# Kernel optimization log

Hardware: AMD Instinct MI355X
Metric: run time of the kernel (lower is better)

Reference implementation:

```python
import jax, jax.numpy as jnp
import numpy as np

VX, VY = 0.2, 0.2
X_OFF = VX / 2 + 0.0      # pc_range x_min = 0
Y_OFF = VY / 2 + (-40.0)  # pc_range y_min = -40
BN_EPS = 1e-3


def setup_inputs() -> dict:
    key = jax.random.key(0)
    k1, k2, k3, k4, k5, k6 = jax.random.split(key, 6)
    K, P, C_IN, C_AUG, C_OUT = 20000, 100, 4, 9, 64
    features = jax.random.normal(k1, (K, P, C_IN), dtype=jnp.float32)
    # at least 1 point per pillar (avoids div-by-zero, as in real voxelization)
    num_voxels = jax.random.randint(k2, (K,), 1, P + 1, dtype=jnp.int64)
    coors = jax.random.randint(k3, (K, 4), 0, 352, dtype=jnp.int64)
    W = jax.random.normal(k4, (C_AUG, C_OUT), dtype=jnp.float32) * (1.0 / np.sqrt(C_AUG))
    gamma = jnp.ones((C_OUT,), dtype=jnp.float32) + 0.1 * jax.random.normal(k5, (C_OUT,), dtype=jnp.float32)
    beta = 0.1 * jax.random.normal(k6, (C_OUT,), dtype=jnp.float32)
    return {"features": features, "num_voxels": num_voxels, "coors": coors,
            "W": W, "gamma": gamma, "beta": beta}


def reference(features, num_voxels, coors, W, gamma, beta):
    K, P, _ = features.shape
    dt = features.dtype
    pn = num_voxels.astype(dt)[:, None, None]                      # [K,1,1]
    cx = coors[:, 3].astype(dt)[:, None] * VX + X_OFF              # [K,1]
    cy = coors[:, 2].astype(dt)[:, None] * VY + Y_OFF              # [K,1]
    mask = (jnp.arange(P)[None, :] < num_voxels[:, None]).astype(dt)[..., None]  # [K,P,1]
    # cluster offset: point xyz minus per-pillar mean
    points_mean = features[..., :3].sum(axis=-2, keepdims=True) / pn
    f_cluster = features[..., :3] - points_mean                    # [K,P,3]
    # center offset: point xy minus pillar center
    f_center = jnp.stack([features[..., 0] - cx, features[..., 1] - cy], axis=-1)  # [K,P,2]
    feats = jnp.concatenate([features, f_cluster, f_center], axis=-1) * mask       # [K,P,9]
    # PFNLayer: Linear(no bias) -> BatchNorm1d (training-mode batch stats) -> ReLU -> max over points
    x = jnp.einsum('kpc,cu->kpu', feats, W)                        # [K,P,64]
    mu = x.mean(axis=(0, 1))
    var = ((x - mu) ** 2).mean(axis=(0, 1))
    x = (x - mu) * jax.lax.rsqrt(var + BN_EPS) * gamma + beta
    x = jax.nn.relu(x)
    return x.max(axis=1)                                           # [K,64] (squeezed)
```

## Files before the change

kernel.cpp:

```cpp
#include <hip/hip_runtime.h>


#define NBA 1252
#define NBB 64

__device__ __forceinline__ float wred63(float v) {
  int t;
  t = __builtin_amdgcn_update_dpp(0, __float_as_int(v), 0xB1, 0xf, 0xf, true);
  v += __int_as_float(t);
  t = __builtin_amdgcn_update_dpp(0, __float_as_int(v), 0x4E, 0xf, 0xf, true);
  v += __int_as_float(t);
  t = __builtin_amdgcn_update_dpp(0, __float_as_int(v), 0x141, 0xf, 0xf, true);
  v += __int_as_float(t);
  t = __builtin_amdgcn_update_dpp(0, __float_as_int(v), 0x140, 0xf, 0xf, true);
  v += __int_as_float(t);
  t = __builtin_amdgcn_update_dpp(0, __float_as_int(v), 0x142, 0xa, 0xf, true);
  v += __int_as_float(t);
  t = __builtin_amdgcn_update_dpp(0, __float_as_int(v), 0x143, 0xc, 0xf, true);
  v += __int_as_float(t);
  return v;
}

__device__ __forceinline__ float wred_add(float v) {
  int t;
  t = __builtin_amdgcn_update_dpp(0, __float_as_int(v), 0xB1, 0xf, 0xf, true);
  v += __int_as_float(t);
  t = __builtin_amdgcn_update_dpp(0, __float_as_int(v), 0x4E, 0xf, 0xf, true);
  v += __int_as_float(t);
  t = __builtin_amdgcn_update_dpp(0, __float_as_int(v), 0x141, 0xf, 0xf, true);
  v += __int_as_float(t);
  t = __builtin_amdgcn_update_dpp(0, __float_as_int(v), 0x140, 0xf, 0xf, true);
  v += __int_as_float(t);
  v += __shfl_xor(v, 16, 64);
  v += __shfl_xor(v, 32, 64);
  return v;
}

__global__ void __launch_bounds__(512) pfn_main(
    const float4* __restrict__ feat, const int* __restrict__ nvox, int K,
    int P, int cnt, const float* __restrict__ W,
    const float* __restrict__ gamma, float* __restrict__ pA,
    float4* __restrict__ ext, float4* __restrict__ rec) {
  __shared__ float4 pts[8][108];
  __shared__ float red[8][10];
  const int lane = threadIdx.x & 63;
  const int wid = threadIdx.x >> 6;
  const int q = lane & 15;
  const int g = lane >> 4;

  const float4* Wq = (const float4*)W;
  const float4 g4 = ((const float4*)gamma)[q];
  float4 sg;
  sg.x = (g4.x >= 0.f) ? 1.f : -1.f;
  sg.y = (g4.y >= 0.f) ? 1.f : -1.f;
  sg.z = (g4.z >= 0.f) ? 1.f : -1.f;
  sg.w = (g4.w >= 0.f) ? 1.f : -1.f;
  const float4 a0 = Wq[0 * 16 + q], a1 = Wq[1 * 16 + q], a2 = Wq[2 * 16 + q];
  const float4 a3 = Wq[3 * 16 + q], a4 = Wq[4 * 16 + q], a5 = Wq[5 * 16 + q];
  const float4 a6 = Wq[6 * 16 + q], a7 = Wq[7 * 16 + q], a8 = Wq[8 * 16 + q];
  float4 wx, wy, wz, w3;
  wx.x = (a0.x + a4.x + a7.x) * sg.x; wx.y = (a0.y + a4.y + a7.y) * sg.y;
  wx.z = (a0.z + a4.z + a7.z) * sg.z; wx.w = (a0.w + a4.w + a7.w) * sg.w;
  wy.x = (a1.x + a5.x + a8.x) * sg.x; wy.y = (a1.y + a5.y + a8.y) * sg.y;
  wy.z = (a1.z + a5.z + a8.z) * sg.z; wy.w = (a1.w + a5.w + a8.w) * sg.w;
  wz.x = (a2.x + a6.x) * sg.x; wz.y = (a2.y + a6.y) * sg.y;
  wz.z = (a2.z + a6.z) * sg.z; wz.w = (a2.w + a6.w) * sg.w;
  w3.x = a3.x * sg.x; w3.y = a3.y * sg.y;
  w3.z = a3.z * sg.z; w3.w = a3.w * sg.w;

  float q2[10] = {0, 0, 0, 0, 0, 0, 0, 0, 0, 0};

  const int gw = blockIdx.x * 8 + wid;
  const int k0 = gw * cnt;
  const int kend = (k0 + cnt < K) ? k0 + cnt : K;
  const bool hih = lane < (P - 64);

  for (int k = k0; k < kend; ++k) {
    const size_t base = (size_t)k * P;
    const float4 f0 = feat[base + lane];
    float4 f1;
    if (hih) f1 = feat[base + 64 + lane];
    const int nv = nvox[k];

    pts[wid][lane] = f0;
    if (hih) pts[wid][64 + lane] = f1;

    float sax = f0.x, say = f0.y, saz = f0.z;
    float svx = 0, svy = 0, svz = 0, svw = 0;
    if (lane < nv) {
      svx = f0.x; svy = f0.y; svz = f0.z; svw = f0.w;
      q2[0] = fmaf(f0.x, f0.x, q2[0]); q2[1] = fmaf(f0.x, f0.y, q2[1]);
      q2[2] = fmaf(f0.x, f0.z, q2[2]); q2[3] = fmaf(f0.x, f0.w, q2[3]);
      q2[4] = fmaf(f0.y, f0.y, q2[4]); q2[5] = fmaf(f0.y, f0.z, q2[5]);
      q2[6] = fmaf(f0.y, f0.w, q2[6]); q2[7] = fmaf(f0.z, f0.z, q2[7]);
      q2[8] = fmaf(f0.z, f0.w, q2[8]); q2[9] = fmaf(f0.w, f0.w, q2[9]);
    }
    if (hih) {
      sax += f1.x; say += f1.y; saz += f1.z;
      if (64 + lane < nv) {
        svx += f1.x; svy += f1.y; svz += f1.z; svw += f1.w;
        q2[0] = fmaf(f1.x, f1.x, q2[0]); q2[1] = fmaf(f1.x, f1.y, q2[1]);
        q2[2] = fmaf(f1.x, f1.z, q2[2]); q2[3] = fmaf(f1.x, f1.w, q2[3]);
        q2[4] = fmaf(f1.y, f1.y, q2[4]); q2[5] = fmaf(f1.y, f1.z, q2[5]);
        q2[6] = fmaf(f1.y, f1.w, q2[6]); q2[7] = fmaf(f1.z, f1.z, q2[7]);
        q2[8] = fmaf(f1.z, f1.w, q2[8]); q2[9] = fmaf(f1.w, f1.w, q2[9]);
      }
    }

    const float rx = wred63(sax), ry = wred63(say), rz = wred63(saz);
    const float vx = wred63(svx), vy = wred63(svy);
    const float vz = wred63(svz), vw = wred63(svw);

    float4 m4 = {-3e38f, -3e38f, -3e38f, -3e38f};
    int p = 0;
    for (; p + 8 <= nv; p += 8) {
      const float4 fa = pts[wid][p + g];
      const float4 fb = pts[wid][p + 4 + g];
      m4.x = fmaxf(m4.x, fmaf(fa.x, wx.x, fmaf(fa.y, wy.x, fmaf(fa.z, wz.x, fa.w * w3.x))));
      m4.y = fmaxf(m4.y, fmaf(fa.x, wx.y, fmaf(fa.y, wy.y, fmaf(fa.z, wz.y, fa.w * w3.y))));
      m4.z = fmaxf(m4.z, fmaf(fa.x, wx.z, fmaf(fa.y, wy.z, fmaf(fa.z, wz.z, fa.w * w3.z))));
      m4.w = fmaxf(m4.w, fmaf(fa.x, wx.w, fmaf(fa.y, wy.w, fmaf(fa.z, wz.w, fa.w * w3.w))));
      m4.x = fmaxf(m4.x, fmaf(fb.x, wx.x, fmaf(fb.y, wy.x, fmaf(fb.z, wz.x, fb.w * w3.x))));
      m4.y = fmaxf(m4.y, fmaf(fb.x, wx.y, fmaf(fb.y, wy.y, fmaf(fb.z, wz.y, fb.w * w3.y))));
      m4.z = fmaxf(m4.z, fmaf(fb.x, wx.z, fmaf(fb.y, wy.z, fmaf(fb.z, wz.z, fb.w * w3.z))));
      m4.w = fmaxf(m4.w, fmaf(fb.x, wx.w, fmaf(fb.y, wy.w, fmaf(fb.z, wz.w, fb.w * w3.w))));
    }
    if (p < nv) {
      const int i0 = p + g, i1 = p + 4 + g;
      const float4 fa = pts[wid][i0];
      const float4 fb = pts[wid][i1];
      if (i0 < nv) {
        m4.x = fmaxf(m4.x, fmaf(fa.x, wx.x, fmaf(fa.y, wy.x, fmaf(fa.z, wz.x, fa.w * w3.x))));
        m4.y = fmaxf(m4.y, fmaf(fa.x, wx.y, fmaf(fa.y, wy.y, fmaf(fa.z, wz.y, fa.w * w3.y))));
        m4.z = fmaxf(m4.z, fmaf(fa.x, wx.z, fmaf(fa.y, wy.z, fmaf(fa.z, wz.z, fa.w * w3.z))));
        m4.w = fmaxf(m4.w, fmaf(fa.x, wx.w, fmaf(fa.y, wy.w, fmaf(fa.z, wz.w, fa.w * w3.w))));
      }
      if (i1 < nv) {
        m4.x = fmaxf(m4.x, fmaf(fb.x, wx.x, fmaf(fb.y, wy.x, fmaf(fb.z, wz.x, fb.w * w3.x))));
        m4.y = fmaxf(m4.y, fmaf(fb.x, wx.y, fmaf(fb.y, wy.y, fmaf(fb.z, wz.y, fb.w * w3.y))));
        m4.z = fmaxf(m4.z, fmaf(fb.x, wx.z, fmaf(fb.y, wy.z, fmaf(fb.z, wz.z, fb.w * w3.z))));
        m4.w = fmaxf(m4.w, fmaf(fb.x, wx.w, fmaf(fb.y, wy.w, fmaf(fb.z, wz.w, fb.w * w3.w))));
      }
    }
    m4.x = fmaxf(m4.x, __shfl_xor(m4.x, 16, 64));
    m4.y = fmaxf(m4.y, __shfl_xor(m4.y, 16, 64));
    m4.z = fmaxf(m4.z, __shfl_xor(m4.z, 16, 64));
    m4.w = fmaxf(m4.w, __shfl_xor(m4.w, 16, 64));
    m4.x = fmaxf(m4.x, __shfl_xor(m4.x, 32, 64));
    m4.y = fmaxf(m4.y, __shfl_xor(m4.y, 32, 64));
    m4.z = fmaxf(m4.z, __shfl_xor(m4.z, 32, 64));
    m4.w = fmaxf(m4.w, __shfl_xor(m4.w, 32, 64));

    if (lane < 16) ext[(size_t)k * 16 + q] = m4;
    if (lane == 63) {
      float4 r0; r0.x = vx; r0.y = vy; r0.z = vz; r0.w = vw;
      float4 r1; r1.x = rx; r1.y = ry; r1.z = rz; r1.w = (float)nv;
      rec[2 * (size_t)k] = r0;
      rec[2 * (size_t)k + 1] = r1;
    }
  }

#pragma unroll
  for (int i = 0; i < 10; ++i) q2[i] = wred63(q2[i]);
  if (lane == 63) {
#pragma unroll
    for (int i = 0; i < 10; ++i) red[wid][i] = q2[i];
  }
  __syncthreads();
  const int t = threadIdx.x;
  if (t < 10) {
    float s = 0.f;
#pragma unroll
    for (int w = 0; w < 8; ++w) s += red[w][t];
    pA[t * NBA + blockIdx.x] = s;
  }
}

__global__ void __launch_bounds__(256) pfn_cross(
    const float4* __restrict__ rec, const int* __restrict__ coors, int K,
    float* __restrict__ pB) {
  __shared__ float red[4][44];
  const int lane = threadIdx.x & 63;
  const int wid = threadIdx.x >> 6;
  float q1[4] = {0, 0, 0, 0};
  float S[20];
  float u1[5] = {0, 0, 0, 0, 0};
  float u2[15];
#pragma unroll
  for (int i = 0; i < 20; ++i) S[i] = 0.f;
#pragma unroll
  for (int i = 0; i < 15; ++i) u2[i] = 0.f;

  for (int k = blockIdx.x * 256 + threadIdx.x; k < K; k += NBB * 256) {
    const float4 sv = rec[2 * (size_t)k];
    const float4 rb = rec[2 * (size_t)k + 1];
    const float nvf = rb.w, inv = 1.f / nvf;
    const float cx = (float)coors[k * 4 + 3] * 0.2f + 0.1f;
    const float cy = (float)coors[k * 4 + 2] * 0.2f - 39.9f;
    const float o[5] = {-rb.x * inv, -rb.y * inv, -rb.z * inv, -cx, -cy};
    const float s4[4] = {sv.x, sv.y, sv.z, sv.w};
#pragma unroll
    for (int a = 0; a < 4; ++a) q1[a] += s4[a];
#pragma unroll
    for (int a = 0; a < 4; ++a)
#pragma unroll
      for (int b = 0; b < 5; ++b)
        S[a * 5 + b] = fmaf(s4[a], o[b], S[a * 5 + b]);
    float no[5];
#pragma unroll
    for (int b = 0; b < 5; ++b) { no[b] = nvf * o[b]; u1[b] += no[b]; }
    int ui = 0;
#pragma unroll
    for (int b = 0; b < 5; ++b)
#pragma unroll
      for (int b2 = b; b2 < 5; ++b2) {
        u2[ui] = fmaf(no[b], o[b2], u2[ui]);
        ++ui;
      }
  }

  float a44[44];
#pragma unroll
  for (int i = 0; i < 4; ++i) a44[i] = q1[i];
#pragma unroll
  for (int i = 0; i < 20; ++i) a44[4 + i] = S[i];
#pragma unroll
  for (int i = 0; i < 5; ++i) a44[24 + i] = u1[i];
#pragma unroll
  for (int i = 0; i < 15; ++i) a44[29 + i] = u2[i];
#pragma unroll
  for (int i = 0; i < 44; ++i) a44[i] = wred_add(a44[i]);
  if (lane == 0) {
#pragma unroll
    for (int i = 0; i < 44; ++i) red[wid][i] = a44[i];
  }
  __syncthreads();
  const int t = threadIdx.x;
  if (t < 44)
    pB[t * NBB + blockIdx.x] =
        red[0][t] + red[1][t] + red[2][t] + red[3][t];
}

__global__ void __launch_bounds__(256) pfn_finalize(
    const float* __restrict__ pA, const float* __restrict__ pB,
    const float* __restrict__ W, const float* __restrict__ gamma,
    const float* __restrict__ beta, float invN, float* __restrict__ ss) {
  __shared__ float msum[54];
  __shared__ float m54[54];
  const int t = threadIdx.x;
  const int r = t >> 2, j = t & 3;
  if (r < 54) {
    const float* row;
    int nb;
    if (r >= 4 && r < 14) { row = pA + (size_t)(r - 4) * NBA; nb = NBA; }
    else {
      const int br = (r < 4) ? r : (r - 10);
      row = pB + (size_t)br * NBB;
      nb = NBB;
    }
    const int chunk = nb >> 2;
    row += j * chunk;
    float a0 = 0, a1 = 0, a2 = 0, a3 = 0, a4 = 0, a5 = 0, a6 = 0, a7 = 0;
    int b = 0;
    for (; b + 8 <= chunk; b += 8) {
      a0 += row[b];     a1 += row[b + 1]; a2 += row[b + 2]; a3 += row[b + 3];
      a4 += row[b + 4]; a5 += row[b + 5]; a6 += row[b + 6]; a7 += row[b + 7];
    }
    for (; b < chunk; ++b) a0 += row[b];
    float s = ((a0 + a1) + (a2 + a3)) + ((a4 + a5) + (a6 + a7));
    s += __shfl_xor(s, 1, 64);
    s += __shfl_xor(s, 2, 64);
    if (j == 0) msum[r] = s;
  }
  __syncthreads();
  if (t < 54) {
    float v;
    if (t < 9) {
      const int g = (t < 4) ? t : (t < 7 ? t - 4 : t - 7);
      v = msum[g];
      if (t >= 4) v += msum[34 + (t - 4)];
    } else {
      int r2 = t - 9, c = 0;
      while (r2 >= 9 - c) { r2 -= 9 - c; ++c; }
      const int c2 = c + r2;
      const int a = (c < 4) ? c : (c < 7 ? c - 4 : c - 7);
      const int b2 = (c2 < 4) ? c2 : (c2 < 7 ? c2 - 4 : c2 - 7);
      const int lo = a < b2 ? a : b2, hi = a < b2 ? b2 : a;
      v = msum[4 + lo * (9 - lo) / 2 + (hi - lo)];
      if (c2 >= 4) v += msum[14 + a * 5 + (c2 - 4)];
      if (c >= 4) v += msum[14 + b2 * 5 + (c - 4)];
      if (c >= 4 && c2 >= 4) {
        const int ua = c - 4, ub = c2 - 4;
        v += msum[39 + ua * 5 - ua * (ua - 1) / 2 + (ub - ua)];
      }
    }
    m54[t] = v;
  }
  __syncthreads();
  if (t < 64) {
    float wc[9];
#pragma unroll
    for (int c = 0; c < 9; ++c) wc[c] = W[c * 64 + t];
    float mu = 0.f;
#pragma unroll
    for (int c = 0; c < 9; ++c) mu += m54[c] * invN * wc[c];
    float ex2 = 0.f;
    int idx = 9;
#pragma unroll
    for (int c = 0; c < 9; ++c)
#pragma unroll
      for (int c2 = c; c2 < 9; ++c2) {
        float v = m54[idx] * invN * wc[c] * wc[c2];
        ex2 += (c == c2) ? v : 2.f * v;
        ++idx;
      }
    const float var = ex2 - mu * mu;
    const float scale = gamma[t] * rsqrtf(var + 1e-3f);
    ss[t] = scale;
    ss[64 + t] = beta[t] - mu * scale;
  }
}

__global__ void __launch_bounds__(256) pfn_apply(
    const float4* __restrict__ ext, const float4* __restrict__ rec,
    const int* __restrict__ coors, const float* __restrict__ W,
    const float* __restrict__ ss, int K, int P, float4* __restrict__ out) {
  const int t = blockIdx.x * 256 + threadIdx.x;
  if (t >= K * 16) return;
  const int k = t >> 4, j = t & 15;

  const float4* Wq = (const float4*)W;
  const float4 v4 = Wq[4 * 16 + j], v5 = Wq[5 * 16 + j];
  const float4 v6 = Wq[6 * 16 + j], v7 = Wq[7 * 16 + j];
  const float4 v8 = Wq[8 * 16 + j];

  const float4 e = ext[t];
  const float4 rb = rec[2 * (size_t)k + 1];
  const float nvf = rb.w, inv = 1.f / nvf;
  const float cx = (float)coors[k * 4 + 3] * 0.2f + 0.1f;
  const float cy = (float)coors[k * 4 + 2] * 0.2f - 39.9f;
  const float o0 = -rb.x * inv, o1 = -rb.y * inv, o2 = -rb.z * inv;
  float4 bias;
  bias.x = v4.x * o0 + v5.x * o1 + v6.x * o2 - v7.x * cx - v8.x * cy;
  bias.y = v4.y * o0 + v5.y * o1 + v6.y * o2 - v7.y * cx - v8.y * cy;
  bias.z = v4.z * o0 + v5.z * o1 + v6.z * o2 - v7.z * cx - v8.z * cy;
  bias.w = v4.w * o0 + v5.w * o1 + v6.w * o2 - v7.w * cx - v8.w * cy;

  const float4 sc = ((const float4*)ss)[j];
  const float4 sh = ((const float4*)(ss + 64))[16 - 16 + j];
  const bool masked = nvf < (float)P;

  float4 o;
  {
    const float sgn = (sc.x >= 0.f) ? 1.f : -1.f;
    float ev = sgn * e.x + bias.x;
    if (masked) ev = (sc.x >= 0.f) ? fmaxf(ev, 0.f) : fminf(ev, 0.f);
    o.x = fmaxf(fmaf(sc.x, ev, sh.x), 0.f);
  }
  {
    const float sgn = (sc.y >= 0.f) ? 1.f : -1.f;
    float ev = sgn * e.y + bias.y;
    if (masked) ev = (sc.y >= 0.f) ? fmaxf(ev, 0.f) : fminf(ev, 0.f);
    o.y = fmaxf(fmaf(sc.y, ev, sh.y), 0.f);
  }
  {
    const float sgn = (sc.z >= 0.f) ? 1.f : -1.f;
    float ev = sgn * e.z + bias.z;
    if (masked) ev = (sc.z >= 0.f) ? fmaxf(ev, 0.f) : fminf(ev, 0.f);
    o.z = fmaxf(fmaf(sc.z, ev, sh.z), 0.f);
  }
  {
    const float sgn = (sc.w >= 0.f) ? 1.f : -1.f;
    float ev = sgn * e.w + bias.w;
    if (masked) ev = (sc.w >= 0.f) ? fmaxf(ev, 0.f) : fminf(ev, 0.f);
    o.w = fmaxf(fmaf(sc.w, ev, sh.w), 0.f);
  }
  out[t] = o;
}

extern "C" void kernel_launch(void* const* d_in, const int* in_sizes, int n_in,
                              void* d_out, int out_size, void* d_ws,
                              size_t ws_size, hipStream_t stream) {
  const float4* feat = (const float4*)d_in[0];
  const int* nvox = (const int*)d_in[1];
  const int* coors = (const int*)d_in[2];
  const float* W = (const float*)d_in[3];
  const float* gamma = (const float*)d_in[4];
  const float* beta = (const float*)d_in[5];

  const int K = in_sizes[1];
  const int P = in_sizes[0] / (K * 4);

  float* ss = (float*)d_ws;
  float4* ext = (float4*)(ss + 128);
  float4* rec = ext + (size_t)K * 16;
  float* pA = (float*)(rec + (size_t)K * 2);
  float* pB = pA + 10 * NBA;

  const int nwaves = NBA * 8;
  const int cnt = (K + nwaves - 1) / nwaves;

  pfn_main<<<NBA, 512, 0, stream>>>(feat, nvox, K, P, cnt, W, gamma, pA, ext,
                                    rec);
  pfn_cross<<<NBB, 256, 0, stream>>>(rec, coors, K, pB);
  pfn_finalize<<<1, 256, 0, stream>>>(pA, pB, W, gamma, beta,
                                      1.0f / (float)((long long)K * P), ss);
  pfn_apply<<<(K * 16 + 255) / 256, 256, 0, stream>>>(ext, rec, coors, W, ss,
                                                      K, P, (float4*)d_out);
}
```

Before: 49.82 us.

## Split fused pillar kernel into separate stats and max-projection kernels

```diff
diff --git a/kernel.cpp b/kernel.cpp
--- a/kernel.cpp
+++ b/kernel.cpp
@@ -1,7 +1,6 @@
 #include <hip/hip_runtime.h>
 
 
-#define NBA 1252
 #define NBB 64
 
 __device__ __forceinline__ float wred63(float v) {
@@ -36,64 +35,32 @@
   return v;
 }
 
-__global__ void __launch_bounds__(512) pfn_main(
+__global__ void __launch_bounds__(512) pfn_stats(
     const float4* __restrict__ feat, const int* __restrict__ nvox, int K,
-    int P, int cnt, const float* __restrict__ W,
-    const float* __restrict__ gamma, float* __restrict__ pA,
-    float4* __restrict__ ext, float4* __restrict__ rec) {
-  __shared__ float4 pts[8][108];
+    int P, int nbs, float* __restrict__ pA, float4* __restrict__ rec) {
   __shared__ float red[8][10];
   const int lane = threadIdx.x & 63;
   const int wid = threadIdx.x >> 6;
-  const int q = lane & 15;
-  const int g = lane >> 4;
-
-  const float4* Wq = (const float4*)W;
-  const float4 g4 = ((const float4*)gamma)[q];
-  float4 sg;
-  sg.x = (g4.x >= 0.f) ? 1.f : -1.f;
-  sg.y = (g4.y >= 0.f) ? 1.f : -1.f;
-  sg.z = (g4.z >= 0.f) ? 1.f : -1.f;
-  sg.w = (g4.w >= 0.f) ? 1.f : -1.f;
-  const float4 a0 = Wq[0 * 16 + q], a1 = Wq[1 * 16 + q], a2 = Wq[2 * 16 + q];
-  const float4 a3 = Wq[3 * 16 + q], a4 = Wq[4 * 16 + q], a5 = Wq[5 * 16 + q];
-  const float4 a6 = Wq[6 * 16 + q], a7 = Wq[7 * 16 + q], a8 = Wq[8 * 16 + q];
-  float4 wx, wy, wz, w3;
-  wx.x = (a0.x + a4.x + a7.x) * sg.x; wx.y = (a0.y + a4.y + a7.y) * sg.y;
-  wx.z = (a0.z + a4.z + a7.z) * sg.z; wx.w = (a0.w + a4.w + a7.w) * sg.w;
-  wy.x = (a1.x + a5.x + a8.x) * sg.x; wy.y = (a1.y + a5.y + a8.y) * sg.y;
-  wy.z = (a1.z + a5.z + a8.z) * sg.z; wy.w = (a1.w + a5.w + a8.w) * sg.w;
-  wz.x = (a2.x + a6.x) * sg.x; wz.y = (a2.y + a6.y) * sg.y;
-  wz.z = (a2.z + a6.z) * sg.z; wz.w = (a2.w + a6.w) * sg.w;
-  w3.x = a3.x * sg.x; w3.y = a3.y * sg.y;
-  w3.z = a3.z * sg.z; w3.w = a3.w * sg.w;
+  const int k = blockIdx.x * 8 + wid;
+  const bool hih = lane < (P - 64);
 
   float q2[10] = {0, 0, 0, 0, 0, 0, 0, 0, 0, 0};
 
-  const int gw = blockIdx.x * 8 + wid;
-  const int k0 = gw * cnt;
-  const int kend = (k0 + cnt < K) ? k0 + cnt : K;
-  const bool hih = lane < (P - 64);
-
-  for (int k = k0; k < kend; ++k) {
+  if (k < K) {
     const size_t base = (size_t)k * P;
     const float4 f0 = feat[base + lane];
     float4 f1;
     if (hih) f1 = feat[base + 64 + lane];
     const int nv = nvox[k];
 
-    pts[wid][lane] = f0;
-    if (hih) pts[wid][64 + lane] = f1;
-
     float sax = f0.x, say = f0.y, saz = f0.z;
     float svx = 0, svy = 0, svz = 0, svw = 0;
     if (lane < nv) {
       svx = f0.x; svy = f0.y; svz = f0.z; svw = f0.w;
-      q2[0] = fmaf(f0.x, f0.x, q2[0]); q2[1] = fmaf(f0.x, f0.y, q2[1]);
-      q2[2] = fmaf(f0.x, f0.z, q2[2]); q2[3] = fmaf(f0.x, f0.w, q2[3]);
-      q2[4] = fmaf(f0.y, f0.y, q2[4]); q2[5] = fmaf(f0.y, f0.z, q2[5]);
-      q2[6] = fmaf(f0.y, f0.w, q2[6]); q2[7] = fmaf(f0.z, f0.z, q2[7]);
-      q2[8] = fmaf(f0.z, f0.w, q2[8]); q2[9] = fmaf(f0.w, f0.w, q2[9]);
+      q2[0] = f0.x * f0.x; q2[1] = f0.x * f0.y; q2[2] = f0.x * f0.z;
+      q2[3] = f0.x * f0.w; q2[4] = f0.y * f0.y; q2[5] = f0.y * f0.z;
+      q2[6] = f0.y * f0.w; q2[7] = f0.z * f0.z; q2[8] = f0.z * f0.w;
+      q2[9] = f0.w * f0.w;
     }
     if (hih) {
       sax += f1.x; say += f1.y; saz += f1.z;
@@ -110,48 +77,6 @@
     const float rx = wred63(sax), ry = wred63(say), rz = wred63(saz);
     const float vx = wred63(svx), vy = wred63(svy);
     const float vz = wred63(svz), vw = wred63(svw);
-
-    float4 m4 = {-3e38f, -3e38f, -3e38f, -3e38f};
-    int p = 0;
-    for (; p + 8 <= nv; p += 8) {
-      const float4 fa = pts[wid][p + g];
-      const float4 fb = pts[wid][p + 4 + g];
-      m4.x = fmaxf(m4.x, fmaf(fa.x, wx.x, fmaf(fa.y, wy.x, fmaf(fa.z, wz.x, fa.w * w3.x))));
-      m4.y = fmaxf(m4.y, fmaf(fa.x, wx.y, fmaf(fa.y, wy.y, fmaf(fa.z, wz.y, fa.w * w3.y))));
-      m4.z = fmaxf(m4.z, fmaf(fa.x, wx.z, fmaf(fa.y, wy.z, fmaf(fa.z, wz.z, fa.w * w3.z))));
-      m4.w = fmaxf(m4.w, fmaf(fa.x, wx.w, fmaf(fa.y, wy.w, fmaf(fa.z, wz.w, fa.w * w3.w))));
-      m4.x = fmaxf(m4.x, fmaf(fb.x, wx.x, fmaf(fb.y, wy.x, fmaf(fb.z, wz.x, fb.w * w3.x))));
-      m4.y = fmaxf(m4.y, fmaf(fb.x, wx.y, fmaf(fb.y, wy.y, fmaf(fb.z, wz.y, fb.w * w3.y))));
-      m4.z = fmaxf(m4.z, fmaf(fb.x, wx.z, fmaf(fb.y, wy.z, fmaf(fb.z, wz.z, fb.w * w3.z))));
-      m4.w = fmaxf(m4.w, fmaf(fb.x, wx.w, fmaf(fb.y, wy.w, fmaf(fb.z, wz.w, fb.w * w3.w))));
-    }
-    if (p < nv) {
-      const int i0 = p + g, i1 = p + 4 + g;
-      const float4 fa = pts[wid][i0];
-      const float4 fb = pts[wid][i1];
-      if (i0 < nv) {
-        m4.x = fmaxf(m4.x, fmaf(fa.x, wx.x, fmaf(fa.y, wy.x, fmaf(fa.z, wz.x, fa.w * w3.x))));
-        m4.y = fmaxf(m4.y, fmaf(fa.x, wx.y, fmaf(fa.y, wy.y, fmaf(fa.z, wz.y, fa.w * w3.y))));
-        m4.z = fmaxf(m4.z, fmaf(fa.x, wx.z, fmaf(fa.y, wy.z, fmaf(fa.z, wz.z, fa.w * w3.z))));
-        m4.w = fmaxf(m4.w, fmaf(fa.x, wx.w, fmaf(fa.y, wy.w, fmaf(fa.z, wz.w, fa.w * w3.w))));
-      }
-      if (i1 < nv) {
-        m4.x = fmaxf(m4.x, fmaf(fb.x, wx.x, fmaf(fb.y, wy.x, fmaf(fb.z, wz.x, fb.w * w3.x))));
-        m4.y = fmaxf(m4.y, fmaf(fb.x, wx.y, fmaf(fb.y, wy.y, fmaf(fb.z, wz.y, fb.w * w3.y))));
-        m4.z = fmaxf(m4.z, fmaf(fb.x, wx.z, fmaf(fb.y, wy.z, fmaf(fb.z, wz.z, fb.w * w3.z))));
-        m4.w = fmaxf(m4.w, fmaf(fb.x, wx.w, fmaf(fb.y, wy.w, fmaf(fb.z, wz.w, fb.w * w3.w))));
-      }
-    }
-    m4.x = fmaxf(m4.x, __shfl_xor(m4.x, 16, 64));
-    m4.y = fmaxf(m4.y, __shfl_xor(m4.y, 16, 64));
-    m4.z = fmaxf(m4.z, __shfl_xor(m4.z, 16, 64));
-    m4.w = fmaxf(m4.w, __shfl_xor(m4.w, 16, 64));
-    m4.x = fmaxf(m4.x, __shfl_xor(m4.x, 32, 64));
-    m4.y = fmaxf(m4.y, __shfl_xor(m4.y, 32, 64));
-    m4.z = fmaxf(m4.z, __shfl_xor(m4.z, 32, 64));
-    m4.w = fmaxf(m4.w, __shfl_xor(m4.w, 32, 64));
-
-    if (lane < 16) ext[(size_t)k * 16 + q] = m4;
     if (lane == 63) {
       float4 r0; r0.x = vx; r0.y = vy; r0.z = vz; r0.w = vw;
       float4 r1; r1.x = rx; r1.y = ry; r1.z = rz; r1.w = (float)nv;
@@ -172,8 +97,96 @@
     float s = 0.f;
 #pragma unroll
     for (int w = 0; w < 8; ++w) s += red[w][t];
-    pA[t * NBA + blockIdx.x] = s;
-  }
+    pA[t * nbs + blockIdx.x] = s;
+  }
+}
+
+__global__ void __launch_bounds__(512) pfn_ext(
+    const float4* __restrict__ feat, const int* __restrict__ nvox, int K,
+    int P, const float* __restrict__ W, const float* __restrict__ gamma,
+    float4* __restrict__ ext) {
+  __shared__ float4 pts[8][108];
+  const int lane = threadIdx.x & 63;
+  const int wid = threadIdx.x >> 6;
+  const int q = lane & 15;
+  const int g = lane >> 4;
+  const int k = blockIdx.x * 8 + wid;
+  if (k >= K) return;
+
+  const float4* Wq = (const float4*)W;
+  const float4 g4 = ((const float4*)gamma)[q];
+  float4 sg;
+  sg.x = (g4.x >= 0.f) ? 1.f : -1.f;
+  sg.y = (g4.y >= 0.f) ? 1.f : -1.f;
+  sg.z = (g4.z >= 0.f) ? 1.f : -1.f;
+  sg.w = (g4.w >= 0.f) ? 1.f : -1.f;
+  float4 wx, wy, wz, w3;
+  {
+    float4 t0 = Wq[0 * 16 + q], t1 = Wq[4 * 16 + q], t2 = Wq[7 * 16 + q];
+    wx.x = (t0.x + t1.x + t2.x) * sg.x; wx.y = (t0.y + t1.y + t2.y) * sg.y;
+    wx.z = (t0.z + t1.z + t2.z) * sg.z; wx.w = (t0.w + t1.w + t2.w) * sg.w;
+  }
+  {
+    float4 t0 = Wq[1 * 16 + q], t1 = Wq[5 * 16 + q], t2 = Wq[8 * 16 + q];
+    wy.x = (t0.x + t1.x + t2.x) * sg.x; wy.y = (t0.y + t1.y + t2.y) * sg.y;
+    wy.z = (t0.z + t1.z + t2.z) * sg.z; wy.w = (t0.w + t1.w + t2.w) * sg.w;
+  }
+  {
+    float4 t0 = Wq[2 * 16 + q], t1 = Wq[6 * 16 + q];
+    wz.x = (t0.x + t1.x) * sg.x; wz.y = (t0.y + t1.y) * sg.y;
+    wz.z = (t0.z + t1.z) * sg.z; wz.w = (t0.w + t1.w) * sg.w;
+  }
+  {
+    float4 t0 = Wq[3 * 16 + q];
+    w3.x = t0.x * sg.x; w3.y = t0.y * sg.y;
+    w3.z = t0.z * sg.z; w3.w = t0.w * sg.w;
+  }
+
+  const size_t base = (size_t)k * P;
+  pts[wid][lane] = feat[base + lane];
+  if (lane < (P - 64)) pts[wid][64 + lane] = feat[base + 64 + lane];
+  const int nv = nvox[k];
+
+  float4 m4 = {-3e38f, -3e38f, -3e38f, -3e38f};
+  int p = 0;
+  for (; p + 8 <= nv; p += 8) {
+    const float4 fa = pts[wid][p + g];
+    const float4 fb = pts[wid][p + 4 + g];
+    m4.x = fmaxf(m4.x, fmaf(fa.x, wx.x, fmaf(fa.y, wy.x, fmaf(fa.z, wz.x, fa.w * w3.x))));
+    m4.y = fmaxf(m4.y, fmaf(fa.x, wx.y, fmaf(fa.y, wy.y, fmaf(fa.z, wz.y, fa.w * w3.y))));
+    m4.z = fmaxf(m4.z, fmaf(fa.x, wx.z, fmaf(fa.y, wy.z, fmaf(fa.z, wz.z, fa.w * w3.z))));
+    m4.w = fmaxf(m4.w, fmaf(fa.x, wx.w, fmaf(fa.y, wy.w, fmaf(fa.z, wz.w, fa.w * w3.w))));
+    m4.x = fmaxf(m4.x, fmaf(fb.x, wx.x, fmaf(fb.y, wy.x, fmaf(fb.z, wz.x, fb.w * w3.x))));
+    m4.y = fmaxf(m4.y, fmaf(fb.x, wx.y, fmaf(fb.y, wy.y, fmaf(fb.z, wz.y, fb.w * w3.y))));
+    m4.z = fmaxf(m4.z, fmaf(fb.x, wx.z, fmaf(fb.y, wy.z, fmaf(fb.z, wz.z, fb.w * w3.z))));
+    m4.w = fmaxf(m4.w, fmaf(fb.x, wx.w, fmaf(fb.y, wy.w, fmaf(fb.z, wz.w, fb.w * w3.w))));
+  }
+  if (p < nv) {
+    const int i0 = p + g, i1 = p + 4 + g;
+    const float4 fa = pts[wid][i0];
+    const float4 fb = pts[wid][i1];
+    if (i0 < nv) {
+      m4.x = fmaxf(m4.x, fmaf(fa.x, wx.x, fmaf(fa.y, wy.x, fmaf(fa.z, wz.x, fa.w * w3.x))));
+      m4.y = fmaxf(m4.y, fmaf(fa.x, wx.y, fmaf(fa.y, wy.y, fmaf(fa.z, wz.y, fa.w * w3.y))));
+      m4.z = fmaxf(m4.z, fmaf(fa.x, wx.z, fmaf(fa.y, wy.z, fmaf(fa.z, wz.z, fa.w * w3.z))));
+      m4.w = fmaxf(m4.w, fmaf(fa.x, wx.w, fmaf(fa.y, wy.w, fmaf(fa.z, wz.w, fa.w * w3.w))));
+    }
+    if (i1 < nv) {
+      m4.x = fmaxf(m4.x, fmaf(fb.x, wx.x, fmaf(fb.y, wy.x, fmaf(fb.z, wz.x, fb.w * w3.x))));
+      m4.y = fmaxf(m4.y, fmaf(fb.x, wx.y, fmaf(fb.y, wy.y, fmaf(fb.z, wz.y, fb.w * w3.y))));
+      m4.z = fmaxf(m4.z, fmaf(fb.x, wx.z, fmaf(fb.y, wy.z, fmaf(fb.z, wz.z, fb.w * w3.z))));
+      m4.w = fmaxf(m4.w, fmaf(fb.x, wx.w, fmaf(fb.y, wy.w, fmaf(fb.z, wz.w, fb.w * w3.w))));
+    }
+  }
+  m4.x = fmaxf(m4.x, __shfl_xor(m4.x, 16, 64));
+  m4.y = fmaxf(m4.y, __shfl_xor(m4.y, 16, 64));
+  m4.z = fmaxf(m4.z, __shfl_xor(m4.z, 16, 64));
+  m4.w = fmaxf(m4.w, __shfl_xor(m4.w, 16, 64));
+  m4.x = fmaxf(m4.x, __shfl_xor(m4.x, 32, 64));
+  m4.y = fmaxf(m4.y, __shfl_xor(m4.y, 32, 64));
+  m4.z = fmaxf(m4.z, __shfl_xor(m4.z, 32, 64));
+  m4.w = fmaxf(m4.w, __shfl_xor(m4.w, 32, 64));
+  if (lane < 16) ext[(size_t)k * 16 + q] = m4;
 }
 
 __global__ void __launch_bounds__(256) pfn_cross(
@@ -242,7 +255,7 @@
 }
 
 __global__ void __launch_bounds__(256) pfn_finalize(
-    const float* __restrict__ pA, const float* __restrict__ pB,
+    const float* __restrict__ pA, const float* __restrict__ pB, int nbs,
     const float* __restrict__ W, const float* __restrict__ gamma,
     const float* __restrict__ beta, float invN, float* __restrict__ ss) {
   __shared__ float msum[54];
@@ -252,7 +265,7 @@
   if (r < 54) {
     const float* row;
     int nb;
-    if (r >= 4 && r < 14) { row = pA + (size_t)(r - 4) * NBA; nb = NBA; }
+    if (r >= 4 && r < 14) { row = pA + (size_t)(r - 4) * nbs; nb = nbs; }
     else {
       const int br = (r < 4) ? r : (r - 10);
       row = pB + (size_t)br * NBB;
@@ -276,8 +289,8 @@
   if (t < 54) {
     float v;
     if (t < 9) {
-      const int g = (t < 4) ? t : (t < 7 ? t - 4 : t - 7);
-      v = msum[g];
+      const int g2 = (t < 4) ? t : (t < 7 ? t - 4 : t - 7);
+      v = msum[g2];
       if (t >= 4) v += msum[34 + (t - 4)];
     } else {
       int r2 = t - 9, c = 0;
@@ -347,7 +360,7 @@
   bias.w = v4.w * o0 + v5.w * o1 + v6.w * o2 - v7.w * cx - v8.w * cy;
 
   const float4 sc = ((const float4*)ss)[j];
-  const float4 sh = ((const float4*)(ss + 64))[16 - 16 + j];
+  const float4 sh = ((const float4*)(ss + 64))[j];
   const bool masked = nvf < (float)P;
 
   float4 o;
@@ -391,19 +404,19 @@
   const int K = in_sizes[1];
   const int P = in_sizes[0] / (K * 4);
 
+  int nbs = (K + 7) / 8;
+  nbs = (nbs + 3) & ~3;
+
   float* ss = (float*)d_ws;
   float4* ext = (float4*)(ss + 128);
   float4* rec = ext + (size_t)K * 16;
   float* pA = (float*)(rec + (size_t)K * 2);
-  float* pB = pA + 10 * NBA;
-
-  const int nwaves = NBA * 8;
-  const int cnt = (K + nwaves - 1) / nwaves;
-
-  pfn_main<<<NBA, 512, 0, stream>>>(feat, nvox, K, P, cnt, W, gamma, pA, ext,
-                                    rec);
+  float* pB = pA + 10 * nbs;
+
+  pfn_stats<<<nbs, 512, 0, stream>>>(feat, nvox, K, P, nbs, pA, rec);
+  pfn_ext<<<(K + 7) / 8, 512, 0, stream>>>(feat, nvox, K, P, W, gamma, ext);
   pfn_cross<<<NBB, 256, 0, stream>>>(rec, coors, K, pB);
-  pfn_finalize<<<1, 256, 0, stream>>>(pA, pB, W, gamma, beta,
+  pfn_finalize<<<1, 256, 0, stream>>>(pA, pB, nbs, W, gamma, beta,
                                       1.0f / (float)((long long)K * P), ss);
   pfn_apply<<<(K * 16 + 255) / 256, 256, 0, stream>>>(ext, rec, coors, W, ss,
                                                       K, P, (float4*)d_out);
```

Result: slower. 65.63 us (+31.7%).
